# Kernel optimization log

Measured on AMD Instinct MI355X. Metric: run time of the kernel, lower is better.

## Reference

```python
import jax, jax.numpy as jnp
import numpy as np

L = 5          # num_layer
D = 300        # emb_dim
N = 100000     # nodes
E = 250000     # edges
G = 4000       # graphs
EPS = 1e-5


def setup_inputs() -> dict:
    key = jax.random.key(0)
    ks = jax.random.split(key, 32)
    f = lambda k, shape, s=0.02: (jax.random.normal(k, shape, dtype=jnp.float32) * s)
    inp = {
        "x_atom": jax.random.randint(ks[0], (N,), 0, 120),
        "x_chir": jax.random.randint(ks[1], (N,), 0, 3),
        "src": jax.random.randint(ks[2], (E,), 0, N),
        "dst": jax.random.randint(ks[3], (E,), 0, N),
        "edge_type": jax.random.randint(ks[4], (E,), 0, 6),
        "edge_dir": jax.random.randint(ks[5], (E,), 0, 3),
        "batch": jnp.sort(jax.random.randint(ks[6], (N,), 0, G)),
        # node feature embeddings
        "x_emb1": f(ks[7], (120, D), 0.1),
        "x_emb2": f(ks[8], (3, D), 0.1),
        # per-layer GIN params (stacked over L)
        "edge_e1": f(ks[9], (L, 6, D), 0.1),
        "edge_e2": f(ks[10], (L, 3, D), 0.1),
        "mlp_w1": f(ks[11], (L, D, 2 * D)),
        "mlp_b1": jnp.zeros((L, 2 * D), jnp.float32),
        "mlp_w2": f(ks[12], (L, 2 * D, D)),
        "mlp_b2": jnp.zeros((L, D), jnp.float32),
        # BatchNorm (inference mode: running stats)
        "bn_gamma": jnp.ones((L, D), jnp.float32),
        "bn_beta": jnp.zeros((L, D), jnp.float32),
        "bn_mean": f(ks[13], (L, D), 0.1),
        "bn_var": jax.random.uniform(ks[14], (L, D), jnp.float32, 0.5, 1.5),
        # virtual node (embedding initialized to zero in the original)
        "vn_emb": jnp.zeros((D,), jnp.float32),
        # vn MLPs: Linear -> LayerNorm -> ReLU -> Linear, L-1 of them
        "vn_w1": f(ks[15], (L - 1, D, D)),
        "vn_b1": jnp.zeros((L - 1, D), jnp.float32),
        "vn_ln_g": jnp.ones((L - 1, D), jnp.float32),
        "vn_ln_b": jnp.zeros((L - 1, D), jnp.float32),
        "vn_w2": f(ks[16], (L - 1, D, D)),
        "vn_b2": jnp.zeros((L - 1, D), jnp.float32),
    }
    return inp


def _forward(x_atom, x_chir, src, dst, edge_type, edge_dir, batch,
             x_emb1, x_emb2, edge_e1, edge_e2, mlp_w1, mlp_b1, mlp_w2, mlp_b2,
             bn_gamma, bn_beta, bn_mean, bn_var,
             vn_emb, vn_w1, vn_b1, vn_ln_g, vn_ln_b, vn_w2, vn_b2):
    n = x_atom.shape[0]
    # node counts per graph for mean pooling (guard empty graphs)
    counts = jnp.maximum(
        jax.ops.segment_sum(jnp.ones((n, 1), jnp.float32), batch, num_segments=G), 1.0)

    h = x_emb1[x_atom] + x_emb2[x_chir]                      # [N, D]
    vn_h = jnp.broadcast_to(vn_emb, (G, D))                  # [G, D]
    h = h + vn_h[batch]

    for l in range(L):
        # --- GIN conv: message = h[src] + edge_emb, scatter-add to dst ---
        edge_emb = edge_e1[l][edge_type] + edge_e2[l][edge_dir]   # [E, D]
        msg = h[src] + edge_emb
        aggr = jax.ops.segment_sum(msg, dst, num_segments=n)      # [N, D]
        # self loops: x_j = h[i], self-loop attr = (type 4, dir 0)
        aggr = aggr + h + (edge_e1[l][4] + edge_e2[l][0])
        # MLP: Linear(D,2D) -> ReLU -> Linear(2D,D)
        z = jax.nn.relu(aggr @ mlp_w1[l] + mlp_b1[l]) @ mlp_w2[l] + mlp_b2[l]
        # BatchNorm1d (eval): running stats
        z = (z - bn_mean[l]) * (bn_gamma[l] * jax.lax.rsqrt(bn_var[l] + EPS)) + bn_beta[l]
        if l < L - 1:
            z = jax.nn.relu(z)  # (dropout is identity at inference)
            # --- virtual node update ---
            pooled = jax.ops.segment_sum(z, batch, num_segments=G) / counts
            vn_new = pooled + vn_h                                # [G, D]
            t = vn_new @ vn_w1[l] + vn_b1[l]
            mu = jnp.mean(t, axis=-1, keepdims=True)
            var = jnp.var(t, axis=-1, keepdims=True)
            t = (t - mu) * jax.lax.rsqrt(var + EPS) * vn_ln_g[l] + vn_ln_b[l]
            vn_h = jax.nn.relu(t) @ vn_w2[l] + vn_b2[l]
            z = z + vn_h[batch]
        h = z
    return h


def reference(x_atom, x_chir, src, dst, edge_type, edge_dir, batch,
              x_emb1, x_emb2, edge_e1, edge_e2, mlp_w1, mlp_b1, mlp_w2, mlp_b2,
              bn_gamma, bn_beta, bn_mean, bn_var,
              vn_emb, vn_w1, vn_b1, vn_ln_g, vn_ln_b, vn_w2, vn_b2):
    return _forward(x_atom, x_chir, src, dst, edge_type, edge_dir, batch,
                    x_emb1, x_emb2, edge_e1, edge_e2, mlp_w1, mlp_b1, mlp_w2, mlp_b2,
                    bn_gamma, bn_beta, bn_mean, bn_var,
                    vn_emb, vn_w1, vn_b1, vn_ln_g, vn_ln_b, vn_w2, vn_b2)
```

## Files before the change

kernel.cpp:

```cpp
#include <hip/hip_runtime.h>

#define DD   300
#define DD2  600
#define GG   4000
#define GPAD 4096
#define LL   5
#define BN_EPS 1e-5f

typedef float f32x4  __attribute__((ext_vector_type(4)));
typedef short bf16x8 __attribute__((ext_vector_type(8)));

__device__ __forceinline__ unsigned short f2bf(float f) {
    unsigned int x = __float_as_uint(f);
    unsigned int r = (x + 0x7FFFu + ((x >> 16) & 1u)) >> 16;
    return (unsigned short)r;
}

__global__ __launch_bounds__(256) void k_hist(const int* __restrict__ idx, int* __restrict__ cnt, int n) {
    int i = blockIdx.x * 256 + threadIdx.x;
    if (i < n) atomicAdd(&cnt[idx[i]], 1);
}

__global__ __launch_bounds__(256) void k_scan1(const int* __restrict__ in, int* __restrict__ bsum, int n) {
    int t = threadIdx.x;
    int i = blockIdx.x * 256 + t;
    int v = (i < n) ? in[i] : 0;
    for (int off = 32; off >= 1; off >>= 1) v += __shfl_down(v, off, 64);
    __shared__ int s[4];
    if ((t & 63) == 0) s[t >> 6] = v;
    __syncthreads();
    if (t == 0) bsum[blockIdx.x] = s[0] + s[1] + s[2] + s[3];
}
__global__ __launch_bounds__(1024) void k_scan2(int* __restrict__ bsum, int nb) {
    __shared__ int s[1024];
    int t = threadIdx.x;
    int v = (t < nb) ? bsum[t] : 0;
    s[t] = v;
    __syncthreads();
    for (int off = 1; off < 1024; off <<= 1) {
        int u = (t >= off) ? s[t - off] : 0;
        __syncthreads();
        s[t] += u;
        __syncthreads();
    }
    if (t < nb) bsum[t] = s[t] - v;
}
__global__ __launch_bounds__(256) void k_scan3(const int* __restrict__ in, const int* __restrict__ boff,
                                               int* __restrict__ out, int n, int total) {
    __shared__ int s[256];
    int t = threadIdx.x;
    int i = blockIdx.x * 256 + t;
    int v = (i < n) ? in[i] : 0;
    s[t] = v;
    __syncthreads();
    for (int off = 1; off < 256; off <<= 1) {
        int u = (t >= off) ? s[t - off] : 0;
        __syncthreads();
        s[t] += u;
        __syncthreads();
    }
    if (i < n) out[i] = boff[blockIdx.x] + s[t] - v;
    if (i == 0) out[n] = total;
}

__global__ __launch_bounds__(256) void k_place(const int* __restrict__ src, const int* __restrict__ dst,
                                               const int* __restrict__ ety, const int* __restrict__ edir,
                                               const int* __restrict__ rowptr, int* __restrict__ cursor,
                                               int* __restrict__ einfo, int E) {
    int e = blockIdx.x * 256 + threadIdx.x;
    if (e >= E) return;
    int d = dst[e];
    int pos = rowptr[d] + atomicAdd(&cursor[d], 1);
    einfo[pos] = src[e] | ((ety[e] * 3 + edir[e]) << 20);
}

__global__ __launch_bounds__(256) void k_comb(const float* __restrict__ e1, const float* __restrict__ e2,
                                              float* __restrict__ comb) {
    int c = blockIdx.x, l = blockIdx.y;
    const float* r1 = e1 + ((size_t)l * 6 + (c / 3)) * DD;
    const float* r2 = e2 + ((size_t)l * 3 + (c % 3)) * DD;
    float* out = comb + ((size_t)l * 18 + c) * DD;
    for (int d = threadIdx.x; d < DD; d += 256) out[d] = r1[d] + r2[d];
}

__global__ __launch_bounds__(256) void k_init_h(const int* __restrict__ xa, const int* __restrict__ xc,
                                                const float* __restrict__ emb1, const float* __restrict__ emb2,
                                                const float* __restrict__ vne,
                                                float* __restrict__ h, int N) {
    int n = blockIdx.x;
    if (n >= N) return;
    int a = xa[n], c = xc[n];
    for (int d = threadIdx.x; d < DD; d += 256)
        h[(size_t)n * DD + d] = emb1[(size_t)a * DD + d] + emb2[(size_t)c * DD + d] + vne[d];
}

__global__ __launch_bounds__(256) void k_init_vn(const float* __restrict__ vne, float* __restrict__ vnh) {
    int g = blockIdx.x;
    for (int d = threadIdx.x; d < DD; d += 256) vnh[(size_t)g * DD + d] = vne[d];
}

__global__ __launch_bounds__(256) void k_aggr(const float* __restrict__ h,
                                              const int* __restrict__ rowptr, const int* __restrict__ einfo,
                                              const float* __restrict__ comb,
                                              const int* __restrict__ batch, const float* __restrict__ vnh,
                                              int use_vn,
                                              unsigned short* __restrict__ aggrb, int N, int Npad) {
    const int node = blockIdx.x * 4 + (threadIdx.x >> 6);
    const int lane = threadIdx.x & 63;
    if (node >= Npad) return;
    unsigned short* out = aggrb + (size_t)node * 320;
    if (node >= N) {
#pragma unroll
        for (int j = 0; j < 5; j++) out[lane + 64 * j] = 0;
        return;
    }
    float acc[5];
    const float* sc = comb + 12 * DD;
    const int p0 = rowptr[node], p1 = rowptr[node + 1];
    if (use_vn) {
        {
            const float* hs = h + (size_t)node * DD;
            const float* vs = vnh + (size_t)batch[node] * DD;
#pragma unroll
            for (int j = 0; j < 5; j++) {
                int d = lane + 64 * j;
                acc[j] = (d < DD) ? hs[d] + sc[d] + vs[d] : 0.f;
            }
        }
        for (int p = p0; p < p1; p++) {
            int info = einfo[p];
            int s = info & 0xFFFFF;
            const float* hr = h + (size_t)s * DD;
            const float* cr = comb + (size_t)(info >> 20) * DD;
            const float* vr = vnh + (size_t)batch[s] * DD;
#pragma unroll
            for (int j = 0; j < 5; j++) {
                int d = lane + 64 * j;
                if (d < DD) acc[j] += hr[d] + cr[d] + vr[d];
            }
        }
    } else {
        {
            const float* hs = h + (size_t)node * DD;
#pragma unroll
            for (int j = 0; j < 5; j++) {
                int d = lane + 64 * j;
                acc[j] = (d < DD) ? hs[d] + sc[d] : 0.f;
            }
        }
        for (int p = p0; p < p1; p++) {
            int info = einfo[p];
            const float* hr = h + (size_t)(info & 0xFFFFF) * DD;
            const float* cr = comb + (size_t)(info >> 20) * DD;
#pragma unroll
            for (int j = 0; j < 5; j++) {
                int d = lane + 64 * j;
                if (d < DD) acc[j] += hr[d] + cr[d];
            }
        }
    }
#pragma unroll
    for (int j = 0; j < 5; j++) {
        int d = lane + 64 * j;
        out[d] = (d < DD) ? f2bf(acc[j]) : (unsigned short)0;
    }
}

__global__ __launch_bounds__(256) void k_convw(const float* __restrict__ w, short* __restrict__ wt,
                                               int K, int Nn, int KP, int NP) {
    int n = blockIdx.x;
    int l = blockIdx.y;
    const float* wl = w + (size_t)l * K * Nn;
    short* wtl = wt + (size_t)l * NP * KP;
    for (int k = threadIdx.x; k < KP; k += 256) {
        float v = (k < K && n < Nn) ? wl[(size_t)k * Nn + n] : 0.f;
        wtl[(size_t)n * KP + k] = (short)f2bf(v);
    }
}

__global__ __launch_bounds__(256) void k_padb(const float* __restrict__ b, float* __restrict__ bp) {
    int l = blockIdx.y;
    int n = blockIdx.x * 256 + threadIdx.x;
    if (n < 640) bp[(size_t)l * 640 + n] = (n < DD2) ? b[(size_t)l * DD2 + n] : 0.f;
}

__global__ __launch_bounds__(256) void k_gemm1(const unsigned short* __restrict__ aggrb,
                                               const short* __restrict__ w1t,
                                               const float* __restrict__ b1p,
                                               unsigned short* __restrict__ hidden) {
    __shared__ short sA[2][64][40];
    __shared__ short sB[2][160][40];
    const int t  = threadIdx.x;
    const int m0 = blockIdx.x * 64;
    const int n0 = blockIdx.y * 160;
    const int ar = t >> 2, aq = (t & 3) << 3;

    {
        *(float4*)&sA[0][ar][aq] = *(const float4*)(aggrb + (size_t)(m0 + ar) * 320 + aq);
#pragma unroll
        for (int i = 0; i < 3; i++) {
            int c = t + (i << 8);
            if (c < 640) {
                int br = c >> 2, bq = (c & 3) << 3;
                *(float4*)&sB[0][br][bq] = *(const float4*)(w1t + (size_t)(n0 + br) * 320 + bq);
            }
        }
    }
    __syncthreads();

    const int lane = t & 63;
    const int w    = t >> 6;
    const int mrow = (w << 4) + (lane & 15);
    const int kb   = (lane >> 4) << 3;
    const int col  = lane & 15;
    const int rq   = (lane >> 4) << 2;

    f32x4 acc[10];
#pragma unroll
    for (int nt = 0; nt < 10; nt++) acc[nt] = (f32x4){0.f, 0.f, 0.f, 0.f};

    for (int ks = 0; ks < 10; ks++) {
        const int nb = ks & 1;
        const bool have = (ks + 1) < 10;
        float4 avr, bv0, bv1, bv2;
        if (have) {
            const int k0 = (ks + 1) << 5;
            avr = *(const float4*)(aggrb + (size_t)(m0 + ar) * 320 + k0 + aq);
            int c = t;
            bv0 = *(const float4*)(w1t + (size_t)(n0 + (c >> 2)) * 320 + k0 + ((c & 3) << 3));
            c = t + 256;
            bv1 = *(const float4*)(w1t + (size_t)(n0 + (c >> 2)) * 320 + k0 + ((c & 3) << 3));
            if (t < 128) {
                c = t + 512;
                bv2 = *(const float4*)(w1t + (size_t)(n0 + (c >> 2)) * 320 + k0 + ((c & 3) << 3));
            }
        }
        bf16x8 a = *(const bf16x8*)&sA[nb][mrow][kb];
#pragma unroll
        for (int nt = 0; nt < 10; nt++) {
            bf16x8 b = *(const bf16x8*)&sB[nb][(nt << 4) + col][kb];
            acc[nt] = __builtin_amdgcn_mfma_f32_16x16x32_bf16(a, b, acc[nt], 0, 0, 0);
        }
        if (have) {
            *(float4*)&sA[nb ^ 1][ar][aq] = avr;
            int c = t;
            *(float4*)&sB[nb ^ 1][c >> 2][(c & 3) << 3] = bv0;
            c = t + 256;
            *(float4*)&sB[nb ^ 1][c >> 2][(c & 3) << 3] = bv1;
            if (t < 128) {
                c = t + 512;
                *(float4*)&sB[nb ^ 1][c >> 2][(c & 3) << 3] = bv2;
            }
        }
        __syncthreads();
    }

#pragma unroll
    for (int nt = 0; nt < 10; nt++) {
        int n = n0 + (nt << 4) + col;
        float bias = b1p[n];
        int mbase = m0 + (w << 4) + rq;
#pragma unroll
        for (int r = 0; r < 4; r++) {
            float vz = fmaxf(acc[nt][r] + bias, 0.f);
            hidden[(size_t)(mbase + r) * 640 + n] = f2bf(vz);
        }
    }
}

__global__ __launch_bounds__(256) void k_gemm2(const unsigned short* __restrict__ hidden,
                                               const short* __restrict__ w2t,
                                               const float* __restrict__ b2,
                                               const float* __restrict__ bng, const float* __restrict__ bnb,
                                               const float* __restrict__ bnm, const float* __restrict__ bnv,
                                               float* __restrict__ h, int N, int relu_out) {
    __shared__ short sA[2][64][40];
    __shared__ short sB[2][160][40];
    const int t  = threadIdx.x;
    const int m0 = blockIdx.x * 64;
    const int n0 = blockIdx.y * 160;
    const int ar = t >> 2, aq = (t & 3) << 3;

    {
        *(float4*)&sA[0][ar][aq] = *(const float4*)(hidden + (size_t)(m0 + ar) * 640 + aq);
#pragma unroll
        for (int i = 0; i < 3; i++) {
            int c = t + (i << 8);
            if (c < 640) {
                int br = c >> 2, bq = (c & 3) << 3;
                *(float4*)&sB[0][br][bq] = *(const float4*)(w2t + (size_t)(n0 + br) * 640 + bq);
            }
        }
    }
    __syncthreads();

    const int lane = t & 63;
    const int w    = t >> 6;
    const int mrow = (w << 4) + (lane & 15);
    const int kb   = (lane >> 4) << 3;
    const int col  = lane & 15;
    const int rq   = (lane >> 4) << 2;

    f32x4 acc[10];
#pragma unroll
    for (int nt = 0; nt < 10; nt++) acc[nt] = (f32x4){0.f, 0.f, 0.f, 0.f};

    for (int ks = 0; ks < 20; ks++) {
        const int nb = ks & 1;
        const bool have = (ks + 1) < 20;
        float4 avr, bv0, bv1, bv2;
        if (have) {
            const int k0 = (ks + 1) << 5;
            avr = *(const float4*)(hidden + (size_t)(m0 + ar) * 640 + k0 + aq);
            int c = t;
            bv0 = *(const float4*)(w2t + (size_t)(n0 + (c >> 2)) * 640 + k0 + ((c & 3) << 3));
            c = t + 256;
            bv1 = *(const float4*)(w2t + (size_t)(n0 + (c >> 2)) * 640 + k0 + ((c & 3) << 3));
            if (t < 128) {
                c = t + 512;
                bv2 = *(const float4*)(w2t + (size_t)(n0 + (c >> 2)) * 640 + k0 + ((c & 3) << 3));
            }
        }
        bf16x8 a = *(const bf16x8*)&sA[nb][mrow][kb];
#pragma unroll
        for (int nt = 0; nt < 10; nt++) {
            bf16x8 b = *(const bf16x8*)&sB[nb][(nt << 4) + col][kb];
            acc[nt] = __builtin_amdgcn_mfma_f32_16x16x32_bf16(a, b, acc[nt], 0, 0, 0);
        }
        if (have) {
            *(float4*)&sA[nb ^ 1][ar][aq] = avr;
            int c = t;
            *(float4*)&sB[nb ^ 1][c >> 2][(c & 3) << 3] = bv0;
            c = t + 256;
            *(float4*)&sB[nb ^ 1][c >> 2][(c & 3) << 3] = bv1;
            if (t < 128) {
                c = t + 512;
                *(float4*)&sB[nb ^ 1][c >> 2][(c & 3) << 3] = bv2;
            }
        }
        __syncthreads();
    }

#pragma unroll
    for (int nt = 0; nt < 10; nt++) {
        int n = n0 + (nt << 4) + col;
        bool nok = (n < DD);
        float bz = 0.f, sc = 1.f, mB = 0.f, bB = 0.f;
        if (nok) {
            bz = b2[n];
            sc = bng[n] * rsqrtf(bnv[n] + BN_EPS);
            mB = bnm[n];
            bB = bnb[n];
        }
        int mbase = m0 + (w << 4) + rq;
#pragma unroll
        for (int r = 0; r < 4; r++) {
            int m = mbase + r;
            if (nok && m < N) {
                float z = (acc[nt][r] + bz - mB) * sc + bB;
                if (relu_out) z = fmaxf(z, 0.f);
                h[(size_t)m * DD + n] = z;
            }
        }
    }
}

__global__ __launch_bounds__(256) void k_pool2(const float* __restrict__ h, const int* __restrict__ gptr,
                                               const float* __restrict__ vnh,
                                               unsigned short* __restrict__ vnin) {
    int g = blockIdx.x, t = threadIdx.x;
    const int gs = gptr[g], ge = gptr[g + 1];
    const float inv = 1.0f / fmaxf((float)(ge - gs), 1.0f);
    const int j0 = t, j1 = t + 256;
    const bool g1 = (j1 < DD);
    float a0 = 0.f, a1 = 0.f;
    for (int n = gs; n < ge; n++) {
        a0 += h[(size_t)n * DD + j0];
        if (g1) a1 += h[(size_t)n * DD + j1];
    }
    vnin[(size_t)g * 320 + j0] = f2bf(a0 * inv + vnh[(size_t)g * DD + j0]);
    if (j1 < 320)
        vnin[(size_t)g * 320 + j1] = g1 ? f2bf(a1 * inv + vnh[(size_t)g * DD + j1]) : (unsigned short)0;
}

__global__ __launch_bounds__(256) void k_vng(const unsigned short* __restrict__ A,
                                             const short* __restrict__ Wt,
                                             const float* __restrict__ bias,
                                             float* __restrict__ outf,
                                             int M) {
    __shared__ short sA[2][64][40];
    __shared__ short sB[2][160][40];
    const int t  = threadIdx.x;
    const int m0 = blockIdx.x * 64;
    const int n0 = blockIdx.y * 160;
    const int ar = t >> 2, aq = (t & 3) << 3;

    {
        *(float4*)&sA[0][ar][aq] = *(const float4*)(A + (size_t)(m0 + ar) * 320 + aq);
#pragma unroll
        for (int i = 0; i < 3; i++) {
            int c = t + (i << 8);
            if (c < 640) {
                int br = c >> 2, bq = (c & 3) << 3;
                *(float4*)&sB[0][br][bq] = *(const float4*)(Wt + (size_t)(n0 + br) * 320 + bq);
            }
        }
    }
    __syncthreads();

    const int lane = t & 63;
    const int w    = t >> 6;
    const int mrow = (w << 4) + (lane & 15);
    const int kb   = (lane >> 4) << 3;
    const int col  = lane & 15;
    const int rq   = (lane >> 4) << 2;

    f32x4 acc[10];
#pragma unroll
    for (int nt = 0; nt < 10; nt++) acc[nt] = (f32x4){0.f, 0.f, 0.f, 0.f};

    for (int ks = 0; ks < 10; ks++) {
        const int nb = ks & 1;
        const bool have = (ks + 1) < 10;
        float4 avr, bv0, bv1, bv2;
        if (have) {
            const int k0 = (ks + 1) << 5;
            avr = *(const float4*)(A + (size_t)(m0 + ar) * 320 + k0 + aq);
            int c = t;
            bv0 = *(const float4*)(Wt + (size_t)(n0 + (c >> 2)) * 320 + k0 + ((c & 3) << 3));
            c = t + 256;
            bv1 = *(const float4*)(Wt + (size_t)(n0 + (c >> 2)) * 320 + k0 + ((c & 3) << 3));
            if (t < 128) {
                c = t + 512;
                bv2 = *(const float4*)(Wt + (size_t)(n0 + (c >> 2)) * 320 + k0 + ((c & 3) << 3));
            }
        }
        bf16x8 a = *(const bf16x8*)&sA[nb][mrow][kb];
#pragma unroll
        for (int nt = 0; nt < 10; nt++) {
            bf16x8 b = *(const bf16x8*)&sB[nb][(nt << 4) + col][kb];
            acc[nt] = __builtin_amdgcn_mfma_f32_16x16x32_bf16(a, b, acc[nt], 0, 0, 0);
        }
        if (have) {
            *(float4*)&sA[nb ^ 1][ar][aq] = avr;
            int c = t;
            *(float4*)&sB[nb ^ 1][c >> 2][(c & 3) << 3] = bv0;
            c = t + 256;
            *(float4*)&sB[nb ^ 1][c >> 2][(c & 3) << 3] = bv1;
            if (t < 128) {
                c = t + 512;
                *(float4*)&sB[nb ^ 1][c >> 2][(c & 3) << 3] = bv2;
            }
        }
        __syncthreads();
    }

#pragma unroll
    for (int nt = 0; nt < 10; nt++) {
        int n = n0 + (nt << 4) + col;
        bool nok = (n < DD);
        float bz = nok ? bias[n] : 0.f;
        int mbase = m0 + (w << 4) + rq;
#pragma unroll
        for (int r = 0; r < 4; r++) {
            int m = mbase + r;
            if (nok && m < M)
                outf[(size_t)m * DD + n] = acc[nt][r] + bz;
        }
    }
}

__global__ __launch_bounds__(256) void k_ln(const float* __restrict__ tbuf,
                                            const float* __restrict__ lng, const float* __restrict__ lnb,
                                            unsigned short* __restrict__ vnrelu) {
    __shared__ float rs[4], rq[4];
    __shared__ float s_mu, s_rstd;
    int g = blockIdx.x, t = threadIdx.x;
    const int j0 = t, j1 = t + 256;
    const bool g1 = (j1 < DD);
    float t0 = tbuf[(size_t)g * DD + j0];
    float t1 = g1 ? tbuf[(size_t)g * DD + j1] : 0.f;
    float ps = t0 + t1;
    float pq = t0 * t0 + t1 * t1;
    for (int off = 32; off >= 1; off >>= 1) { ps += __shfl_down(ps, off, 64); pq += __shfl_down(pq, off, 64); }
    int wid = t >> 6, lane = t & 63;
    if (lane == 0) { rs[wid] = ps; rq[wid] = pq; }
    __syncthreads();
    if (t == 0) {
        float S = rs[0] + rs[1] + rs[2] + rs[3];
        float Q = rq[0] + rq[1] + rq[2] + rq[3];
        float mu = S / DD;
        float var = Q / DD - mu * mu;
        s_mu = mu;
        s_rstd = rsqrtf(var + BN_EPS);
    }
    __syncthreads();
    float mu = s_mu, rstd = s_rstd;
    float r0 = fmaxf((t0 - mu) * rstd * lng[j0] + lnb[j0], 0.f);
    vnrelu[(size_t)g * 320 + j0] = f2bf(r0);
    if (j1 < 320) {
        float r1 = g1 ? fmaxf((t1 - mu) * rstd * lng[j1] + lnb[j1], 0.f) : 0.f;
        vnrelu[(size_t)g * 320 + j1] = g1 ? f2bf(r1) : (unsigned short)0;
    }
}

extern "C" void kernel_launch(void* const* d_in, const int* in_sizes, int n_in,
                              void* d_out, int out_size, void* d_ws, size_t ws_size,
                              hipStream_t stream) {
    const int*   x_atom = (const int*)d_in[0];
    const int*   x_chir = (const int*)d_in[1];
    const int*   src    = (const int*)d_in[2];
    const int*   dst    = (const int*)d_in[3];
    const int*   ety    = (const int*)d_in[4];
    const int*   edir   = (const int*)d_in[5];
    const int*   batch  = (const int*)d_in[6];
    const float* emb1   = (const float*)d_in[7];
    const float* emb2   = (const float*)d_in[8];
    const float* e1     = (const float*)d_in[9];
    const float* e2     = (const float*)d_in[10];
    const float* w1     = (const float*)d_in[11];
    const float* b1     = (const float*)d_in[12];
    const float* w2     = (const float*)d_in[13];
    const float* b2     = (const float*)d_in[14];
    const float* bng    = (const float*)d_in[15];
    const float* bnb    = (const float*)d_in[16];
    const float* bnm    = (const float*)d_in[17];
    const float* bnv    = (const float*)d_in[18];
    const float* vne    = (const float*)d_in[19];
    const float* vw1    = (const float*)d_in[20];
    const float* vb1    = (const float*)d_in[21];
    const float* lng    = (const float*)d_in[22];
    const float* lnb    = (const float*)d_in[23];
    const float* vw2    = (const float*)d_in[24];
    const float* vb2    = (const float*)d_in[25];

    const int N = in_sizes[0];
    const int E = in_sizes[2];
    const int gx = (N + 63) / 64;
    const int Npad = gx * 64;
    const int nbN = (N + 255) / 256;
    const int nbG = (GG + 255) / 256;

    float* h = (float*)d_out;

    unsigned short* aggrb  = (unsigned short*)d_ws;
    unsigned short* hidden = aggrb + (size_t)Npad * 320;
    short*          w1t    = (short*)(hidden + (size_t)Npad * 640);
    short*          w2t    = w1t + (size_t)LL * 640 * 320;
    short*          vw1t   = w2t + (size_t)LL * 320 * 640;
    short*          vw2t   = vw1t + (size_t)(LL - 1) * 320 * 320;
    unsigned short* vnin   = (unsigned short*)(vw2t + (size_t)(LL - 1) * 320 * 320);
    unsigned short* vnrelu = vnin + (size_t)GPAD * 320;
    float*          b1p    = (float*)(vnrelu + (size_t)GPAD * 320);
    float*          comb   = b1p + (size_t)LL * 640;
    float*          tbuf   = comb + (size_t)LL * 18 * DD;
    float*          vnh    = tbuf + (size_t)GG * DD;
    int*            deg    = (int*)(vnh + (size_t)GG * DD);
    int*            cursor = deg + N;
    int*            gcnt   = cursor + N;
    int*            rowptr = gcnt + GG;
    int*            gptr   = rowptr + (N + 1);
    int*            bsumN  = gptr + (GG + 1);
    int*            bsumG  = bsumN + 1024;
    int*            einfo  = bsumG + 1024;

    k_convw<<<dim3(640, LL), 256, 0, stream>>>(w1, w1t, DD, DD2, 320, 640);
    k_convw<<<dim3(320, LL), 256, 0, stream>>>(w2, w2t, DD2, DD, 640, 320);
    k_convw<<<dim3(320, LL - 1), 256, 0, stream>>>(vw1, vw1t, DD, DD, 320, 320);
    k_convw<<<dim3(320, LL - 1), 256, 0, stream>>>(vw2, vw2t, DD, DD, 320, 320);
    k_padb<<<dim3(3, LL), 256, 0, stream>>>(b1, b1p);
    k_comb<<<dim3(18, LL), 256, 0, stream>>>(e1, e2, comb);

    hipMemsetAsync(deg, 0, (size_t)(2 * N + GG) * sizeof(int), stream);
    k_hist<<<(E + 255) / 256, 256, 0, stream>>>(dst, deg, E);
    k_hist<<<(N + 255) / 256, 256, 0, stream>>>(batch, gcnt, N);
    k_scan1<<<nbN, 256, 0, stream>>>(deg, bsumN, N);
    k_scan2<<<1, 1024, 0, stream>>>(bsumN, nbN);
    k_scan3<<<nbN, 256, 0, stream>>>(deg, bsumN, rowptr, N, E);
    k_scan1<<<nbG, 256, 0, stream>>>(gcnt, bsumG, GG);
    k_scan2<<<1, 1024, 0, stream>>>(bsumG, nbG);
    k_scan3<<<nbG, 256, 0, stream>>>(gcnt, bsumG, gptr, GG, N);
    k_place<<<(E + 255) / 256, 256, 0, stream>>>(src, dst, ety, edir, rowptr, cursor, einfo, E);

    k_init_h<<<N, 256, 0, stream>>>(x_atom, x_chir, emb1, emb2, vne, h, N);
    k_init_vn<<<GG, 256, 0, stream>>>(vne, vnh);

    for (int l = 0; l < LL; l++) {
        k_aggr<<<Npad / 4, 256, 0, stream>>>(h, rowptr, einfo, comb + (size_t)l * 18 * DD,
                                             batch, vnh, (l > 0) ? 1 : 0, aggrb, N, Npad);
        k_gemm1<<<dim3(gx, 4), 256, 0, stream>>>(aggrb, w1t + (size_t)l * 640 * 320,
                                                 b1p + (size_t)l * 640, hidden);
        k_gemm2<<<dim3(gx, 2), 256, 0, stream>>>(hidden, w2t + (size_t)l * 320 * 640,
                                                 b2 + (size_t)l * DD,
                                                 bng + (size_t)l * DD, bnb + (size_t)l * DD,
                                                 bnm + (size_t)l * DD, bnv + (size_t)l * DD,
                                                 h, N, (l < LL - 1) ? 1 : 0);
        if (l < LL - 1) {
            k_pool2<<<GG, 256, 0, stream>>>(h, gptr, vnh, vnin);
            k_vng<<<dim3(GPAD / 64, 2), 256, 0, stream>>>(vnin, vw1t + (size_t)l * 320 * 320,
                                                          vb1 + (size_t)l * DD, tbuf, GG);
            k_ln<<<GG, 256, 0, stream>>>(tbuf, lng + (size_t)l * DD, lnb + (size_t)l * DD, vnrelu);
            k_vng<<<dim3(GPAD / 64, 2), 256, 0, stream>>>(vnrelu, vw2t + (size_t)l * 320 * 320,
                                                          vb2 + (size_t)l * DD, vnh, GG);
        }
    }
}
```

Measured before the change: 2.178 ms.

## Fuse both MLP GEMMs into one kernel keeping hidden tile in LDS

Replaces the two separate GEMM kernels with one fused k_mlp kernel per 64-row tile. The A operand is held in registers, and the hidden activations are computed in 160-column chunks into shared memory, then consumed right away by the second GEMM, accumulating all 320 output columns. This removes the global round trip of the bf16 hidden buffer and one launch per layer. In exchange, each block now does the whole N dimension with fewer blocks, more registers (20 accumulators plus 10 A fragments), and more shared memory, which can lower occupancy.

New measurement: 2.126 ms. 2.4% less time.

```diff
diff --git a/kernel.cpp b/kernel.cpp
--- a/kernel.cpp
+++ b/kernel.cpp
@@ -184,182 +184,122 @@
     if (n < 640) bp[(size_t)l * 640 + n] = (n < DD2) ? b[(size_t)l * DD2 + n] : 0.f;
 }
 
-__global__ __launch_bounds__(256) void k_gemm1(const unsigned short* __restrict__ aggrb,
-                                               const short* __restrict__ w1t,
-                                               const float* __restrict__ b1p,
-                                               unsigned short* __restrict__ hidden) {
-    __shared__ short sA[2][64][40];
+
+#define LD3(PTR, STRIDE, ROWBASE, KOFF)                                                                     \
+    do {                                                                                                    \
+        v0 = *(const float4*)((PTR) + (size_t)((ROWBASE) + (t >> 2)) * (STRIDE) + (KOFF) + (t & 3) * 8);    \
+        v1 = *(const float4*)((PTR) + (size_t)((ROWBASE) + (t >> 2) + 64) * (STRIDE) + (KOFF) + (t & 3) * 8); \
+        if (t < 128)                                                                                        \
+            v2 = *(const float4*)((PTR) + (size_t)((ROWBASE) + (t >> 2) + 128) * (STRIDE) + (KOFF) + (t & 3) * 8); \
+    } while (0)
+
+#define ST3(BUF)                                                    \
+    do {                                                            \
+        *(float4*)&sB[BUF][t >> 2][(t & 3) * 8] = v0;               \
+        *(float4*)&sB[BUF][(t >> 2) + 64][(t & 3) * 8] = v1;        \
+        if (t < 128) *(float4*)&sB[BUF][(t >> 2) + 128][(t & 3) * 8] = v2; \
+    } while (0)
+
+__global__ __launch_bounds__(256, 2) void k_mlp(const unsigned short* __restrict__ aggrb,
+                                                const short* __restrict__ w1t,
+                                                const float* __restrict__ b1p,
+                                                const short* __restrict__ w2t,
+                                                const float* __restrict__ b2,
+                                                const float* __restrict__ bng, const float* __restrict__ bnb,
+                                                const float* __restrict__ bnm, const float* __restrict__ bnv,
+                                                float* __restrict__ h, int N, int relu_out) {
+    __shared__ short sH[64][168];
     __shared__ short sB[2][160][40];
-    const int t  = threadIdx.x;
-    const int m0 = blockIdx.x * 64;
-    const int n0 = blockIdx.y * 160;
-    const int ar = t >> 2, aq = (t & 3) << 3;
-
-    {
-        *(float4*)&sA[0][ar][aq] = *(const float4*)(aggrb + (size_t)(m0 + ar) * 320 + aq);
-#pragma unroll
-        for (int i = 0; i < 3; i++) {
-            int c = t + (i << 8);
-            if (c < 640) {
-                int br = c >> 2, bq = (c & 3) << 3;
-                *(float4*)&sB[0][br][bq] = *(const float4*)(w1t + (size_t)(n0 + br) * 320 + bq);
-            }
-        }
-    }
-    __syncthreads();
-
+
+    const int t    = threadIdx.x;
+    const int m0   = blockIdx.x * 64;
     const int lane = t & 63;
     const int w    = t >> 6;
-    const int mrow = (w << 4) + (lane & 15);
-    const int kb   = (lane >> 4) << 3;
     const int col  = lane & 15;
-    const int rq   = (lane >> 4) << 2;
-
-    f32x4 acc[10];
-#pragma unroll
-    for (int nt = 0; nt < 10; nt++) acc[nt] = (f32x4){0.f, 0.f, 0.f, 0.f};
-
-    for (int ks = 0; ks < 10; ks++) {
-        const int nb = ks & 1;
-        const bool have = (ks + 1) < 10;
-        float4 avr, bv0, bv1, bv2;
-        if (have) {
-            const int k0 = (ks + 1) << 5;
-            avr = *(const float4*)(aggrb + (size_t)(m0 + ar) * 320 + k0 + aq);
-            int c = t;
-            bv0 = *(const float4*)(w1t + (size_t)(n0 + (c >> 2)) * 320 + k0 + ((c & 3) << 3));
-            c = t + 256;
-            bv1 = *(const float4*)(w1t + (size_t)(n0 + (c >> 2)) * 320 + k0 + ((c & 3) << 3));
-            if (t < 128) {
-                c = t + 512;
-                bv2 = *(const float4*)(w1t + (size_t)(n0 + (c >> 2)) * 320 + k0 + ((c & 3) << 3));
-            }
-        }
-        bf16x8 a = *(const bf16x8*)&sA[nb][mrow][kb];
-#pragma unroll
-        for (int nt = 0; nt < 10; nt++) {
-            bf16x8 b = *(const bf16x8*)&sB[nb][(nt << 4) + col][kb];
-            acc[nt] = __builtin_amdgcn_mfma_f32_16x16x32_bf16(a, b, acc[nt], 0, 0, 0);
-        }
-        if (have) {
-            *(float4*)&sA[nb ^ 1][ar][aq] = avr;
-            int c = t;
-            *(float4*)&sB[nb ^ 1][c >> 2][(c & 3) << 3] = bv0;
-            c = t + 256;
-            *(float4*)&sB[nb ^ 1][c >> 2][(c & 3) << 3] = bv1;
-            if (t < 128) {
-                c = t + 512;
-                *(float4*)&sB[nb ^ 1][c >> 2][(c & 3) << 3] = bv2;
-            }
-        }
-        __syncthreads();
-    }
-
-#pragma unroll
-    for (int nt = 0; nt < 10; nt++) {
-        int n = n0 + (nt << 4) + col;
-        float bias = b1p[n];
-        int mbase = m0 + (w << 4) + rq;
-#pragma unroll
-        for (int r = 0; r < 4; r++) {
-            float vz = fmaxf(acc[nt][r] + bias, 0.f);
-            hidden[(size_t)(mbase + r) * 640 + n] = f2bf(vz);
-        }
-    }
-}
-
-__global__ __launch_bounds__(256) void k_gemm2(const unsigned short* __restrict__ hidden,
-                                               const short* __restrict__ w2t,
-                                               const float* __restrict__ b2,
-                                               const float* __restrict__ bng, const float* __restrict__ bnb,
-                                               const float* __restrict__ bnm, const float* __restrict__ bnv,
-                                               float* __restrict__ h, int N, int relu_out) {
-    __shared__ short sA[2][64][40];
-    __shared__ short sB[2][160][40];
-    const int t  = threadIdx.x;
-    const int m0 = blockIdx.x * 64;
-    const int n0 = blockIdx.y * 160;
-    const int ar = t >> 2, aq = (t & 3) << 3;
-
+    const int kq   = lane >> 4;
+    const int kb   = kq << 3;
+    const int mrow = (w << 4) + col;
+
+    bf16x8 areg[10];
     {
-        *(float4*)&sA[0][ar][aq] = *(const float4*)(hidden + (size_t)(m0 + ar) * 640 + aq);
-#pragma unroll
-        for (int i = 0; i < 3; i++) {
-            int c = t + (i << 8);
-            if (c < 640) {
-                int br = c >> 2, bq = (c & 3) << 3;
-                *(float4*)&sB[0][br][bq] = *(const float4*)(w2t + (size_t)(n0 + br) * 640 + bq);
-            }
-        }
-    }
-    __syncthreads();
-
-    const int lane = t & 63;
-    const int w    = t >> 6;
-    const int mrow = (w << 4) + (lane & 15);
-    const int kb   = (lane >> 4) << 3;
-    const int col  = lane & 15;
-    const int rq   = (lane >> 4) << 2;
-
-    f32x4 acc[10];
-#pragma unroll
-    for (int nt = 0; nt < 10; nt++) acc[nt] = (f32x4){0.f, 0.f, 0.f, 0.f};
-
-    for (int ks = 0; ks < 20; ks++) {
-        const int nb = ks & 1;
-        const bool have = (ks + 1) < 20;
-        float4 avr, bv0, bv1, bv2;
-        if (have) {
-            const int k0 = (ks + 1) << 5;
-            avr = *(const float4*)(hidden + (size_t)(m0 + ar) * 640 + k0 + aq);
-            int c = t;
-            bv0 = *(const float4*)(w2t + (size_t)(n0 + (c >> 2)) * 640 + k0 + ((c & 3) << 3));
-            c = t + 256;
-            bv1 = *(const float4*)(w2t + (size_t)(n0 + (c >> 2)) * 640 + k0 + ((c & 3) << 3));
-            if (t < 128) {
-                c = t + 512;
-                bv2 = *(const float4*)(w2t + (size_t)(n0 + (c >> 2)) * 640 + k0 + ((c & 3) << 3));
-            }
-        }
-        bf16x8 a = *(const bf16x8*)&sA[nb][mrow][kb];
-#pragma unroll
-        for (int nt = 0; nt < 10; nt++) {
-            bf16x8 b = *(const bf16x8*)&sB[nb][(nt << 4) + col][kb];
-            acc[nt] = __builtin_amdgcn_mfma_f32_16x16x32_bf16(a, b, acc[nt], 0, 0, 0);
-        }
-        if (have) {
-            *(float4*)&sA[nb ^ 1][ar][aq] = avr;
-            int c = t;
-            *(float4*)&sB[nb ^ 1][c >> 2][(c & 3) << 3] = bv0;
-            c = t + 256;
-            *(float4*)&sB[nb ^ 1][c >> 2][(c & 3) << 3] = bv1;
-            if (t < 128) {
-                c = t + 512;
-                *(float4*)&sB[nb ^ 1][c >> 2][(c & 3) << 3] = bv2;
-            }
-        }
-        __syncthreads();
-    }
-
-#pragma unroll
-    for (int nt = 0; nt < 10; nt++) {
-        int n = n0 + (nt << 4) + col;
-        bool nok = (n < DD);
-        float bz = 0.f, sc = 1.f, mB = 0.f, bB = 0.f;
-        if (nok) {
-            bz = b2[n];
-            sc = bng[n] * rsqrtf(bnv[n] + BN_EPS);
-            mB = bnm[n];
-            bB = bnb[n];
-        }
-        int mbase = m0 + (w << 4) + rq;
-#pragma unroll
-        for (int r = 0; r < 4; r++) {
-            int m = mbase + r;
-            if (nok && m < N) {
-                float z = (acc[nt][r] + bz - mB) * sc + bB;
-                if (relu_out) z = fmaxf(z, 0.f);
-                h[(size_t)m * DD + n] = z;
+        const unsigned short* ap = aggrb + (size_t)(m0 + mrow) * 320 + kb;
+#pragma unroll
+        for (int ks = 0; ks < 10; ks++)
+            areg[ks] = *(const bf16x8*)(ap + ks * 32);
+        float4 v0, v1, v2;
+        LD3(w1t, 320, 0, 0);
+        ST3(0);
+    }
+    __syncthreads();
+
+    f32x4 zacc[20];
+#pragma unroll
+    for (int j = 0; j < 20; j++) zacc[j] = (f32x4){0.f, 0.f, 0.f, 0.f};
+
+    for (int ch = 0; ch < 4; ch++) {
+        f32x4 hacc[10];
+#pragma unroll
+        for (int j = 0; j < 10; j++) hacc[j] = (f32x4){0.f, 0.f, 0.f, 0.f};
+
+#pragma unroll
+        for (int ks = 0; ks < 10; ks++) {
+            float4 v0, v1, v2;
+            if (ks < 9) LD3(w1t, 320, ch * 160, (ks + 1) * 32);
+            else        LD3(w2t, 640, 0, ch * 160);
+#pragma unroll
+            for (int nt = 0; nt < 10; nt++) {
+                bf16x8 b = *(const bf16x8*)&sB[ks & 1][(nt << 4) + col][kb];
+                hacc[nt] = __builtin_amdgcn_mfma_f32_16x16x32_bf16(areg[ks], b, hacc[nt], 0, 0, 0);
+            }
+            ST3((ks & 1) ^ 1);
+            if (ks == 9) {
+#pragma unroll
+                for (int nt = 0; nt < 10; nt++) {
+                    float bias = b1p[ch * 160 + (nt << 4) + col];
+#pragma unroll
+                    for (int r = 0; r < 4; r++)
+                        sH[(w << 4) + (kq << 2) + r][(nt << 4) + col] =
+                            (short)f2bf(fmaxf(hacc[nt][r] + bias, 0.f));
+                }
+            }
+            __syncthreads();
+        }
+
+#pragma unroll
+        for (int s = 0; s < 10; s++) {
+            const int ks2 = s >> 1, half = s & 1;
+            float4 v0, v1, v2;
+            bool stage = true;
+            if (s < 9)       LD3(w2t, 640, ((s + 1) & 1) * 160, ch * 160 + ((s + 1) >> 1) * 32);
+            else if (ch < 3) LD3(w1t, 320, (ch + 1) * 160, 0);
+            else stage = false;
+            bf16x8 a = *(const bf16x8*)&sH[mrow][ks2 * 32 + kb];
+#pragma unroll
+            for (int jt = 0; jt < 10; jt++) {
+                bf16x8 b = *(const bf16x8*)&sB[s & 1][(jt << 4) + col][kb];
+                zacc[half * 10 + jt] = __builtin_amdgcn_mfma_f32_16x16x32_bf16(a, b, zacc[half * 10 + jt], 0, 0, 0);
+            }
+            if (stage) ST3((s & 1) ^ 1);
+            __syncthreads();
+        }
+    }
+
+#pragma unroll
+    for (int j = 0; j < 20; j++) {
+        int n = (j << 4) + col;
+        if (n < DD) {
+            float bz = b2[n];
+            float sc = bng[n] * rsqrtf(bnv[n] + BN_EPS);
+            float mB = bnm[n], bB = bnb[n];
+            int mbase = m0 + (w << 4) + (kq << 2);
+#pragma unroll
+            for (int r = 0; r < 4; r++) {
+                int m = mbase + r;
+                if (m < N) {
+                    float z = (zacc[j][r] + bz - mB) * sc + bB;
+                    if (relu_out) z = fmaxf(z, 0.f);
+                    h[(size_t)m * DD + n] = z;
+                }
             }
         }
     }
@@ -588,13 +528,13 @@
     for (int l = 0; l < LL; l++) {
         k_aggr<<<Npad / 4, 256, 0, stream>>>(h, rowptr, einfo, comb + (size_t)l * 18 * DD,
                                              batch, vnh, (l > 0) ? 1 : 0, aggrb, N, Npad);
-        k_gemm1<<<dim3(gx, 4), 256, 0, stream>>>(aggrb, w1t + (size_t)l * 640 * 320,
-                                                 b1p + (size_t)l * 640, hidden);
-        k_gemm2<<<dim3(gx, 2), 256, 0, stream>>>(hidden, w2t + (size_t)l * 320 * 640,
-                                                 b2 + (size_t)l * DD,
-                                                 bng + (size_t)l * DD, bnb + (size_t)l * DD,
-                                                 bnm + (size_t)l * DD, bnv + (size_t)l * DD,
-                                                 h, N, (l < LL - 1) ? 1 : 0);
+        k_mlp<<<gx, 256, 0, stream>>>(aggrb, w1t + (size_t)l * 640 * 320,
+                                      b1p + (size_t)l * 640,
+                                      w2t + (size_t)l * 320 * 640,
+                                      b2 + (size_t)l * DD,
+                                      bng + (size_t)l * DD, bnb + (size_t)l * DD,
+                                      bnm + (size_t)l * DD, bnv + (size_t)l * DD,
+                                      h, N, (l < LL - 1) ? 1 : 0);
         if (l < LL - 1) {
             k_pool2<<<GG, 256, 0, stream>>>(h, gptr, vnh, vnin);
             k_vng<<<dim3(GPAD / 64, 2), 256, 0, stream>>>(vnin, vw1t + (size_t)l * 320 * 320,
```
